# Kernel optimization log

Hardware: AMD Instinct MI355X
Metric: run time of the kernel (lower is better)

Reference implementation:

```python
import jax, jax.numpy as jnp
import numpy as np

H = 8          # kv heads
D = 128        # head dim
EPS = 1e-6
NEG = -1e9

def rmsnorm(x, w):
    rms = jnp.sqrt(jnp.mean(x * x, axis=-1, keepdims=True) + EPS)
    return x / rms * w

def apply_rotary(x, cos, sin):
    # x: [B, h, T, D]; cos/sin: [1, 1, T, D/2]
    x1, x2 = jnp.split(x, 2, axis=-1)
    return jnp.concatenate([x1 * cos - x2 * sin, x1 * sin + x2 * cos], axis=-1)


def setup_inputs() -> dict:
    key = jax.random.key(0)
    ks = jax.random.split(key, 7)
    B, T, hid = 1, 4096, 1024
    s = 0.02
    return {
        "x":   jax.random.normal(ks[0], (B, T, hid), jnp.float32),
        "cos": jax.random.normal(ks[1], (1, 1, T, D // 2), jnp.float32),
        "sin": jax.random.normal(ks[2], (1, 1, T, D // 2), jnp.float32),
        "Wq":  jax.random.normal(ks[3], (hid, 2 * hid), jnp.float32) * s,
        "Wk":  jax.random.normal(ks[4], (hid, hid), jnp.float32) * s,
        "Wv":  jax.random.normal(ks[5], (hid, hid), jnp.float32) * s,
        "Wo":  jax.random.normal(ks[6], (2 * hid, hid), jnp.float32) * s,
        "qn_w": jnp.ones((D,), jnp.float32),
        "kn_w": jnp.ones((D,), jnp.float32),
    }


def reference(x, cos, sin, Wq, Wk, Wv, Wo, qn_w, kn_w):
    B, T, _ = x.shape
    scale = D ** -0.5

    q = (x @ Wq).reshape(B, T, 2 * H, D).transpose(0, 2, 1, 3)  # [B,2H,T,D]
    k = (x @ Wk).reshape(B, T, H, D).transpose(0, 2, 1, 3)      # [B,H,T,D]
    v = (x @ Wv).reshape(B, T, H, D).transpose(0, 2, 1, 3)      # [B,H,T,D]

    q = apply_rotary(rmsnorm(q, qn_w), cos, sin)
    k = apply_rotary(rmsnorm(k, kn_w), cos, sin)

    # GQA expand: query head i uses kv head i // 2
    k = jnp.repeat(k, 2, axis=1)  # [B,2H,T,D]
    v = jnp.repeat(v, 2, axis=1)

    attn = jnp.einsum("bhtd,bhsd->bhts", q, k) * scale
    causal = jnp.tril(jnp.ones((T, T), bool))
    attn = jnp.where(causal, attn, NEG)
    attn = jax.nn.softmax(attn, axis=-1)

    out = jnp.einsum("bhts,bhsd->bhtd", attn, v)
    out = out.transpose(0, 2, 1, 3).reshape(B, T, 2 * H * D)
    return out @ Wo
```

## Files before the change

### kernel.cpp

```cpp
#include <hip/hip_runtime.h>
#include <hip/hip_bf16.h>

#define H2 16
#define HKV 8
#define DHEAD 128
#define HID 1024
#define NQ 2048

typedef unsigned short u16;
typedef __bf16 bf16x8 __attribute__((ext_vector_type(8)));
typedef float f32x4 __attribute__((ext_vector_type(4)));

__device__ __forceinline__ u16 f2bf(float x) {
    unsigned int u = __float_as_uint(x);
    unsigned int r = (u + 0x7fffu + ((u >> 16) & 1u)) >> 16;
    return (u16)r;
}

__device__ __forceinline__ unsigned int pack_bf16(float hi, float lo) {
    unsigned int a = __float_as_uint(hi) + 0x8000u;
    unsigned int b = __float_as_uint(lo) + 0x8000u;
    return __builtin_amdgcn_perm(a, b, 0x07060302u);
}

__device__ __forceinline__ bf16x8 ld_frag(const u16* p) {
    bf16x8 r;
    *reinterpret_cast<uint4*>(&r) = *reinterpret_cast<const uint4*>(p);
    return r;
}

__device__ __forceinline__ void gload_lds16(const u16* g, u16* l) {
    __builtin_amdgcn_global_load_lds((const __attribute__((address_space(1))) void*)g,
                                     (__attribute__((address_space(3))) void*)l, 16, 0, 0);
}

__global__ __launch_bounds__(256) void cast_f32_bf16(const float* __restrict__ in,
                                                     u16* __restrict__ out, int n4) {
    int i = blockIdx.x * 256 + threadIdx.x;
    if (i < n4) {
        float4 v = reinterpret_cast<const float4*>(in)[i];
        ushort4 o;
        o.x = f2bf(v.x); o.y = f2bf(v.y); o.z = f2bf(v.z); o.w = f2bf(v.w);
        reinterpret_cast<ushort4*>(out)[i] = o;
    }
}

__global__ __launch_bounds__(256) void transpose_cast(const float* __restrict__ in,
                                                      u16* __restrict__ out, int K, int N) {
    __shared__ u16 t[32][34];
    int k0 = blockIdx.x * 32, n0 = blockIdx.y * 32;
    for (int c = threadIdx.x; c < 1024; c += 256) {
        int k = c >> 5, n = c & 31;
        t[k][n] = f2bf(in[(size_t)(k0 + k) * N + n0 + n]);
    }
    __syncthreads();
    for (int c = threadIdx.x; c < 1024; c += 256) {
        int n = c >> 5, k = c & 31;
        out[(size_t)(n0 + n) * K + k0 + k] = t[k][n];
    }
}

__global__ __launch_bounds__(256) void gemm_bf16(const u16* __restrict__ A,
                                                 const u16* __restrict__ Bt,
                                                 float* __restrict__ C,
                                                 int M, int N, int K) {
    __shared__ u16 As[128 * 32];
    __shared__ u16 Bs[128 * 32];
    int tid = threadIdx.x;
    int lane = tid & 63, wave = tid >> 6;
    int quad = lane >> 4, l15 = lane & 15;
    int wr = wave >> 1, wc = wave & 1;
    int m0 = blockIdx.y * 128, n0 = blockIdx.x * 128;

    f32x4 zero = {0.f, 0.f, 0.f, 0.f};
    f32x4 acc[4][4];
    for (int i = 0; i < 4; i++)
        for (int j = 0; j < 4; j++) acc[i][j] = zero;

    int r0 = 16 * wave + (lane >> 2);
    int r1 = r0 + 64;
    int ks0 = (lane & 3) ^ ((r0 >> 1) & 3);
    int ks1 = (lane & 3) ^ ((r1 >> 1) & 3);
    const u16* ga0 = A + (size_t)(m0 + r0) * K + ks0 * 8;
    const u16* ga1 = A + (size_t)(m0 + r1) * K + ks1 * 8;
    const u16* gb0 = Bt + (size_t)(n0 + r0) * K + ks0 * 8;
    const u16* gb1 = Bt + (size_t)(n0 + r1) * K + ks1 * 8;
    u16* la0 = &As[wave * 512];
    u16* la1 = &As[(wave + 4) * 512];
    u16* lb0 = &Bs[wave * 512];
    u16* lb1 = &Bs[(wave + 4) * 512];

    int swz = (quad ^ ((l15 >> 1) & 3)) * 8;

    for (int k0 = 0; k0 < K; k0 += 32) {
        __syncthreads();
        gload_lds16(ga0 + k0, la0);
        gload_lds16(ga1 + k0, la1);
        gload_lds16(gb0 + k0, lb0);
        gload_lds16(gb1 + k0, lb1);
        __syncthreads();
        bf16x8 a[4], b[4];
        #pragma unroll
        for (int i = 0; i < 4; i++) a[i] = ld_frag(&As[(64 * wr + 16 * i + l15) * 32 + swz]);
        #pragma unroll
        for (int j = 0; j < 4; j++) b[j] = ld_frag(&Bs[(64 * wc + 16 * j + l15) * 32 + swz]);
        #pragma unroll
        for (int i = 0; i < 4; i++)
            #pragma unroll
            for (int j = 0; j < 4; j++)
                acc[i][j] = __builtin_amdgcn_mfma_f32_16x16x32_bf16(a[i], b[j], acc[i][j], 0, 0, 0);
    }
    for (int i = 0; i < 4; i++) {
        int rowb = m0 + 64 * wr + 16 * i + quad * 4;
        for (int j = 0; j < 4; j++) {
            int col = n0 + 64 * wc + 16 * j + l15;
            for (int r = 0; r < 4; r++)
                C[(size_t)(rowb + r) * N + col] = acc[i][j][r];
        }
    }
}

__global__ __launch_bounds__(256) void norm_rope(const float* __restrict__ raw,
                                                 const float* __restrict__ cosp,
                                                 const float* __restrict__ sinp,
                                                 const float* __restrict__ w,
                                                 u16* __restrict__ out,
                                                 int T, int nh, int rowstride, int coloff,
                                                 float outscale) {
    int wave = threadIdx.x >> 6, lane = threadIdx.x & 63;
    int wid = blockIdx.x * 4 + wave;
    int t = wid / nh, h = wid % nh;
    if (t >= T) return;
    const float* r = raw + (size_t)t * rowstride + coloff + h * 128;
    float v1 = r[lane], v2 = r[lane + 64];
    float ss = v1 * v1 + v2 * v2;
    for (int off = 1; off < 64; off <<= 1) ss += __shfl_xor(ss, off);
    float inv = rsqrtf(ss * (1.f / 128.f) + 1e-6f);
    float n1 = v1 * inv * w[lane], n2 = v2 * inv * w[lane + 64];
    float c = cosp[(size_t)t * 64 + lane], s = sinp[(size_t)t * 64 + lane];
    float o1 = (n1 * c - n2 * s) * outscale;
    float o2 = (n1 * s + n2 * c) * outscale;
    u16* op = out + ((size_t)h * T + t) * 128;
    op[lane] = f2bf(o1);
    op[lane + 64] = f2bf(o2);
}

__global__ __launch_bounds__(256) void v_transpose(const float* __restrict__ vraw,
                                                   u16* __restrict__ Vbt, int T) {
    __shared__ u16 tt[128][72];
    int h = blockIdx.y, t0 = blockIdx.x * 64;
    for (int c = threadIdx.x; c < 8192; c += 256) {
        int r = c >> 7, d = c & 127;
        tt[d][r] = f2bf(vraw[(size_t)(t0 + r) * 4096 + 3072 + h * 128 + d]);
    }
    __syncthreads();
    for (int c = threadIdx.x; c < 8192; c += 256) {
        int d = c >> 6, r = c & 63;
        Vbt[((size_t)h * 128 + d) * T + t0 + r] = tt[d][r];
    }
}

__global__ __launch_bounds__(256) void flash_attn(const u16* __restrict__ Qb,
                                                  const u16* __restrict__ Kb,
                                                  const u16* __restrict__ Vbt,
                                                  u16* __restrict__ attn, int T) {
    __shared__ u16 Ks[2][64 * 128];
    __shared__ u16 Vt[2][128 * 64];
    __shared__ u16 Ps[64 * 64];
    int tid = threadIdx.x;
    int lane = tid & 63, wave = tid >> 6;
    int quad = lane >> 4, l15 = lane & 15;
    int swb8 = (l15 & 7) * 8;
    int h = blockIdx.y;
    int j = (int)blockIdx.x;
    int kvh = h >> 1;

    const u16* kbase = Kb + (size_t)kvh * T * 128;
    const u16* vbase = Vbt + (size_t)kvh * 128 * T;

    int krow_ = (lane >> 4);
    int kseg_ = (lane & 15);
    int vrow_ = (lane >> 3);
    int vseg_ = (lane & 7);

    auto stage = [&](int s0, int b) {
        #pragma unroll
        for (int i = 0; i < 4; i++) {
            int ch = wave * 4 + i;
            int r = ch * 4 + krow_;
            int s = kseg_ ^ (r & 7);
            gload_lds16(kbase + (size_t)(s0 + r) * 128 + s * 8, &Ks[b][ch * 512]);
        }
        #pragma unroll
        for (int i = 0; i < 4; i++) {
            int ch = wave * 4 + i;
            int d = ch * 8 + vrow_;
            int s = vseg_ ^ (d & 7);
            gload_lds16(vbase + (size_t)d * T + s0 + s * 8, &Vt[b][ch * 512]);
        }
    };

    bf16x8 onesf;
    #pragma unroll
    for (int i = 0; i < 8; i++) onesf[i] = (__bf16)1.0f;
    f32x4 zero = {0.f, 0.f, 0.f, 0.f};
    const float L2E = 1.44269504f;

    for (int pass = 0; pass < 2; ++pass) {
        int qt = pass == 0 ? (63 - j) : j;
        int q0 = qt * 64;

        bf16x8 qf[4];
        {
            const u16* qp = Qb + ((size_t)h * T + q0 + 16 * wave + l15) * 128 + quad * 8;
            #pragma unroll
            for (int kk = 0; kk < 4; kk++) qf[kk] = ld_frag(qp + kk * 32);
        }

        float m_i = -3.0e38f;
        f32x4 lsum = zero;
        f32x4 o[8];
        for (int dt = 0; dt < 8; dt++) o[dt] = zero;

        int ntiles = qt + 1;
        stage(0, 0);
        __syncthreads();

        for (int it = 0; it < ntiles; ++it) {
            int b = it & 1;
            if (it + 1 < ntiles) stage((it + 1) * 64, 1 - b);
            int s0 = it * 64;

            f32x4 scT[4];
            for (int jt = 0; jt < 4; jt++) scT[jt] = zero;
            #pragma unroll
            for (int kk = 0; kk < 4; kk++)
                #pragma unroll
                for (int jt = 0; jt < 4; jt++) {
                    bf16x8 kfrag = ld_frag(&Ks[b][(jt * 16 + l15) * 128 + ((kk * 32 + quad * 8) ^ swb8)]);
                    scT[jt] = __builtin_amdgcn_mfma_f32_16x16x32_bf16(kfrag, qf[kk], scT[jt], 0, 0, 0);
                }

            if (s0 == q0) {
                int qloc = 16 * wave + l15;
                #pragma unroll
                for (int jt = 0; jt < 4; jt++)
                    for (int r = 0; r < 4; r++)
                        if (jt * 16 + quad * 4 + r > qloc) scT[jt][r] = -1e30f;
            }

            float mt = scT[0][0];
            #pragma unroll
            for (int jt = 0; jt < 4; jt++)
                for (int r = 0; r < 4; r++) mt = fmaxf(mt, scT[jt][r]);
            mt = fmaxf(mt, __shfl_xor(mt, 16));
            mt = fmaxf(mt, __shfl_xor(mt, 32));
            float mnew = fmaxf(m_i, mt);
            float alpha = __expf(m_i - mnew);
            m_i = mnew;
            float mls = mnew * L2E;

            #pragma unroll
            for (int jt = 0; jt < 4; jt++)
                for (int r = 0; r < 4; r++)
                    scT[jt][r] = exp2f(fmaf(scT[jt][r], L2E, -mls));

            {
                int prow = 16 * wave + l15;
                #pragma unroll
                for (int jt = 0; jt < 4; jt++) {
                    int s8 = 2 * jt + (quad >> 1);
                    uint2 wv;
                    wv.x = pack_bf16(scT[jt][1], scT[jt][0]);
                    wv.y = pack_bf16(scT[jt][3], scT[jt][2]);
                    *reinterpret_cast<uint2*>(&Ps[prow * 64 + (s8 ^ (l15 & 7)) * 8 + (quad & 1) * 4]) = wv;
                }
            }

            float av[4];
            #pragma unroll
            for (int r = 0; r < 4; r++) av[r] = __shfl(alpha, quad * 4 + r);
            #pragma unroll
            for (int r = 0; r < 4; r++) lsum[r] *= av[r];
            #pragma unroll
            for (int dt = 0; dt < 8; dt++)
                for (int r = 0; r < 4; r++) o[dt][r] *= av[r];

            asm volatile("s_waitcnt lgkmcnt(0)" ::: "memory");

            #pragma unroll
            for (int kk2 = 0; kk2 < 2; kk2++) {
                bf16x8 pa = ld_frag(&Ps[(16 * wave + l15) * 64 + (((4 * kk2 + quad) ^ (l15 & 7)) * 8)]);
                lsum = __builtin_amdgcn_mfma_f32_16x16x32_bf16(pa, onesf, lsum, 0, 0, 0);
                #pragma unroll
                for (int dt = 0; dt < 8; dt++) {
                    bf16x8 vb = ld_frag(&Vt[b][(dt * 16 + l15) * 64 + ((kk2 * 32 + quad * 8) ^ swb8)]);
                    o[dt] = __builtin_amdgcn_mfma_f32_16x16x32_bf16(pa, vb, o[dt], 0, 0, 0);
                }
            }
            __syncthreads();
        }

        float inv[4];
        for (int r = 0; r < 4; r++) inv[r] = 1.f / lsum[r];
        for (int dt = 0; dt < 8; dt++)
            for (int r = 0; r < 4; r++) {
                int row = q0 + 16 * wave + quad * 4 + r;
                attn[(size_t)row * NQ + h * DHEAD + dt * 16 + l15] = f2bf(o[dt][r] * inv[r]);
            }
    }
}

extern "C" void kernel_launch(void* const* d_in, const int* in_sizes, int n_in,
                              void* d_out, int out_size, void* d_ws, size_t ws_size,
                              hipStream_t stream) {
    const float* x    = (const float*)d_in[0];
    const float* cosp = (const float*)d_in[1];
    const float* sinp = (const float*)d_in[2];
    const float* Wq   = (const float*)d_in[3];
    const float* Wk   = (const float*)d_in[4];
    const float* Wv   = (const float*)d_in[5];
    const float* Wo   = (const float*)d_in[6];
    const float* qnw  = (const float*)d_in[7];
    const float* knw  = (const float*)d_in[8];
    float* out = (float*)d_out;
    const int T = in_sizes[1] / 64;

    char* ws = (char*)d_ws;
    size_t off = 0;
    auto alloc = [&](size_t bytes) {
        char* p = ws + off;
        off += (bytes + 255) & ~(size_t)255;
        return p;
    };
    u16*   xb     = (u16*)alloc((size_t)T * HID * 2);
    u16*   Wqkvb  = (u16*)alloc((size_t)4096 * HID * 2);
    u16*   Wob    = (u16*)alloc((size_t)HID * NQ * 2);
    float* qkvraw = (float*)alloc((size_t)T * 4096 * 4);
    u16*   Qb     = (u16*)alloc((size_t)H2 * T * DHEAD * 2);
    u16*   Kb     = (u16*)alloc((size_t)HKV * T * DHEAD * 2);
    u16*   Vbt    = (u16*)alloc((size_t)HKV * DHEAD * T * 2);
    u16*   attn   = (u16*)alloc((size_t)T * NQ * 2);

    cast_f32_bf16<<<(T * HID / 4 + 255) / 256, 256, 0, stream>>>(x, xb, T * HID / 4);
    transpose_cast<<<dim3(HID / 32, NQ / 32), 256, 0, stream>>>(Wq, Wqkvb, HID, NQ);
    transpose_cast<<<dim3(HID / 32, HID / 32), 256, 0, stream>>>(Wk, Wqkvb + (size_t)2048 * HID, HID, HID);
    transpose_cast<<<dim3(HID / 32, HID / 32), 256, 0, stream>>>(Wv, Wqkvb + (size_t)3072 * HID, HID, HID);
    transpose_cast<<<dim3(NQ / 32, HID / 32), 256, 0, stream>>>(Wo, Wob, NQ, HID);

    gemm_bf16<<<dim3(4096 / 128, T / 128), 256, 0, stream>>>(xb, Wqkvb, qkvraw, T, 4096, HID);

    const float scale = 0.08838834764831845f;
    norm_rope<<<T * H2 / 4, 256, 0, stream>>>(qkvraw, cosp, sinp, qnw, Qb, T, H2, 4096, 0, scale);
    norm_rope<<<T * HKV / 4, 256, 0, stream>>>(qkvraw, cosp, sinp, knw, Kb, T, HKV, 4096, 2048, 1.0f);
    v_transpose<<<dim3(T / 64, HKV), 256, 0, stream>>>(qkvraw, Vbt, T);

    flash_attn<<<dim3(32, H2), 256, 0, stream>>>(Qb, Kb, Vbt, attn, T);

    gemm_bf16<<<dim3(HID / 128, T / 128), 256, 0, stream>>>(attn, Wob, out, T, HID, NQ);
}
```

Baseline: 377.5 us.

## Emit bf16 QKV, merge norm/rope and weight casts, use 64-wide output GEMM tiles

The QKV projection now writes bf16 instead of fp32, which halves intermediate traffic. The downstream norm/rope and V transpose read bf16 directly, and the Q and K norm_rope launches are merged into one kernel. The Wk and Wv transpose-casts are fused into a single launch. The output projection uses a 128x64 tile so the N=1024 GEMM gets more blocks for better CU occupancy. Rounding QKV to bf16 before RMSNorm adds a small precision loss.

```diff
diff --git a/kernel.cpp b/kernel.cpp
--- a/kernel.cpp
+++ b/kernel.cpp
@@ -15,6 +15,9 @@
     unsigned int u = __float_as_uint(x);
     unsigned int r = (u + 0x7fffu + ((u >> 16) & 1u)) >> 16;
     return (u16)r;
+}
+__device__ __forceinline__ float bf2f(u16 x) {
+    return __uint_as_float(((unsigned int)x) << 16);
 }
 
 __device__ __forceinline__ unsigned int pack_bf16(float hi, float lo) {
@@ -48,6 +51,25 @@
 __global__ __launch_bounds__(256) void transpose_cast(const float* __restrict__ in,
                                                       u16* __restrict__ out, int K, int N) {
     __shared__ u16 t[32][34];
+    int k0 = blockIdx.x * 32, n0 = blockIdx.y * 32;
+    for (int c = threadIdx.x; c < 1024; c += 256) {
+        int k = c >> 5, n = c & 31;
+        t[k][n] = f2bf(in[(size_t)(k0 + k) * N + n0 + n]);
+    }
+    __syncthreads();
+    for (int c = threadIdx.x; c < 1024; c += 256) {
+        int n = c >> 5, k = c & 31;
+        out[(size_t)(n0 + n) * K + k0 + k] = t[k][n];
+    }
+}
+
+__global__ __launch_bounds__(256) void transpose_cast2(const float* __restrict__ inA,
+                                                       const float* __restrict__ inB,
+                                                       u16* __restrict__ outA,
+                                                       u16* __restrict__ outB, int K, int N) {
+    __shared__ u16 t[32][34];
+    const float* in = blockIdx.z ? inB : inA;
+    u16* out = blockIdx.z ? outB : outA;
     int k0 = blockIdx.x * 32, n0 = blockIdx.y * 32;
     for (int c = threadIdx.x; c < 1024; c += 256) {
         int k = c >> 5, n = c & 31;
@@ -120,19 +142,144 @@
     }
 }
 
-__global__ __launch_bounds__(256) void norm_rope(const float* __restrict__ raw,
-                                                 const float* __restrict__ cosp,
-                                                 const float* __restrict__ sinp,
-                                                 const float* __restrict__ w,
-                                                 u16* __restrict__ out,
-                                                 int T, int nh, int rowstride, int coloff,
-                                                 float outscale) {
+__global__ __launch_bounds__(256) void gemm_bf16_ob(const u16* __restrict__ A,
+                                                    const u16* __restrict__ Bt,
+                                                    u16* __restrict__ C,
+                                                    int M, int N, int K) {
+    __shared__ u16 As[128 * 32];
+    __shared__ u16 Bs[128 * 32];
+    int tid = threadIdx.x;
+    int lane = tid & 63, wave = tid >> 6;
+    int quad = lane >> 4, l15 = lane & 15;
+    int wr = wave >> 1, wc = wave & 1;
+    int m0 = blockIdx.y * 128, n0 = blockIdx.x * 128;
+
+    f32x4 zero = {0.f, 0.f, 0.f, 0.f};
+    f32x4 acc[4][4];
+    for (int i = 0; i < 4; i++)
+        for (int j = 0; j < 4; j++) acc[i][j] = zero;
+
+    int r0 = 16 * wave + (lane >> 2);
+    int r1 = r0 + 64;
+    int ks0 = (lane & 3) ^ ((r0 >> 1) & 3);
+    int ks1 = (lane & 3) ^ ((r1 >> 1) & 3);
+    const u16* ga0 = A + (size_t)(m0 + r0) * K + ks0 * 8;
+    const u16* ga1 = A + (size_t)(m0 + r1) * K + ks1 * 8;
+    const u16* gb0 = Bt + (size_t)(n0 + r0) * K + ks0 * 8;
+    const u16* gb1 = Bt + (size_t)(n0 + r1) * K + ks1 * 8;
+    u16* la0 = &As[wave * 512];
+    u16* la1 = &As[(wave + 4) * 512];
+    u16* lb0 = &Bs[wave * 512];
+    u16* lb1 = &Bs[(wave + 4) * 512];
+
+    int swz = (quad ^ ((l15 >> 1) & 3)) * 8;
+
+    for (int k0 = 0; k0 < K; k0 += 32) {
+        __syncthreads();
+        gload_lds16(ga0 + k0, la0);
+        gload_lds16(ga1 + k0, la1);
+        gload_lds16(gb0 + k0, lb0);
+        gload_lds16(gb1 + k0, lb1);
+        __syncthreads();
+        bf16x8 a[4], b[4];
+        #pragma unroll
+        for (int i = 0; i < 4; i++) a[i] = ld_frag(&As[(64 * wr + 16 * i + l15) * 32 + swz]);
+        #pragma unroll
+        for (int j = 0; j < 4; j++) b[j] = ld_frag(&Bs[(64 * wc + 16 * j + l15) * 32 + swz]);
+        #pragma unroll
+        for (int i = 0; i < 4; i++)
+            #pragma unroll
+            for (int j = 0; j < 4; j++)
+                acc[i][j] = __builtin_amdgcn_mfma_f32_16x16x32_bf16(a[i], b[j], acc[i][j], 0, 0, 0);
+    }
+    for (int i = 0; i < 4; i++) {
+        int rowb = m0 + 64 * wr + 16 * i + quad * 4;
+        for (int j = 0; j < 4; j++) {
+            int col = n0 + 64 * wc + 16 * j + l15;
+            for (int r = 0; r < 4; r++)
+                C[(size_t)(rowb + r) * N + col] = f2bf(acc[i][j][r]);
+        }
+    }
+}
+
+__global__ __launch_bounds__(256) void gemm_bf16_n64(const u16* __restrict__ A,
+                                                     const u16* __restrict__ Bt,
+                                                     float* __restrict__ C,
+                                                     int M, int N, int K) {
+    __shared__ u16 As[128 * 32];
+    __shared__ u16 Bs[64 * 32];
+    int tid = threadIdx.x;
+    int lane = tid & 63, wave = tid >> 6;
+    int quad = lane >> 4, l15 = lane & 15;
+    int m0 = blockIdx.y * 128, n0 = blockIdx.x * 64;
+
+    f32x4 zero = {0.f, 0.f, 0.f, 0.f};
+    f32x4 acc[2][4];
+    for (int i = 0; i < 2; i++)
+        for (int j = 0; j < 4; j++) acc[i][j] = zero;
+
+    int ra0 = 32 * wave + (lane >> 2);
+    int ra1 = ra0 + 16;
+    int rb  = 16 * wave + (lane >> 2);
+    int ksa0 = (lane & 3) ^ ((ra0 >> 1) & 3);
+    int ksa1 = (lane & 3) ^ ((ra1 >> 1) & 3);
+    int ksb  = (lane & 3) ^ ((rb >> 1) & 3);
+    const u16* ga0 = A + (size_t)(m0 + ra0) * K + ksa0 * 8;
+    const u16* ga1 = A + (size_t)(m0 + ra1) * K + ksa1 * 8;
+    const u16* gb  = Bt + (size_t)(n0 + rb) * K + ksb * 8;
+    u16* la0 = &As[(2 * wave) * 512];
+    u16* la1 = &As[(2 * wave + 1) * 512];
+    u16* lb  = &Bs[wave * 512];
+
+    int swz = (quad ^ ((l15 >> 1) & 3)) * 8;
+
+    for (int k0 = 0; k0 < K; k0 += 32) {
+        __syncthreads();
+        gload_lds16(ga0 + k0, la0);
+        gload_lds16(ga1 + k0, la1);
+        gload_lds16(gb + k0, lb);
+        __syncthreads();
+        bf16x8 a[2], b[4];
+        #pragma unroll
+        for (int i = 0; i < 2; i++) a[i] = ld_frag(&As[(32 * wave + 16 * i + l15) * 32 + swz]);
+        #pragma unroll
+        for (int j = 0; j < 4; j++) b[j] = ld_frag(&Bs[(16 * j + l15) * 32 + swz]);
+        #pragma unroll
+        for (int i = 0; i < 2; i++)
+            #pragma unroll
+            for (int j = 0; j < 4; j++)
+                acc[i][j] = __builtin_amdgcn_mfma_f32_16x16x32_bf16(a[i], b[j], acc[i][j], 0, 0, 0);
+    }
+    for (int i = 0; i < 2; i++) {
+        int rowb = m0 + 32 * wave + 16 * i + quad * 4;
+        for (int j = 0; j < 4; j++) {
+            int col = n0 + 16 * j + l15;
+            for (int r = 0; r < 4; r++)
+                C[(size_t)(rowb + r) * N + col] = acc[i][j][r];
+        }
+    }
+}
+
+__global__ __launch_bounds__(256) void norm_rope_qk(const u16* __restrict__ qkv,
+                                                    const float* __restrict__ cosp,
+                                                    const float* __restrict__ sinp,
+                                                    const float* __restrict__ qnw,
+                                                    const float* __restrict__ knw,
+                                                    u16* __restrict__ Qb,
+                                                    u16* __restrict__ Kb,
+                                                    int T, float qscale) {
     int wave = threadIdx.x >> 6, lane = threadIdx.x & 63;
     int wid = blockIdx.x * 4 + wave;
-    int t = wid / nh, h = wid % nh;
+    int t = wid / 24, unit = wid % 24;
     if (t >= T) return;
-    const float* r = raw + (size_t)t * rowstride + coloff + h * 128;
-    float v1 = r[lane], v2 = r[lane + 64];
+    bool isq = unit < 16;
+    int coloff = isq ? unit * 128 : 2048 + (unit - 16) * 128;
+    const float* w = isq ? qnw : knw;
+    float outscale = isq ? qscale : 1.0f;
+    u16* out = isq ? (Qb + ((size_t)unit * T + t) * 128)
+                   : (Kb + ((size_t)(unit - 16) * T + t) * 128);
+    const u16* r = qkv + (size_t)t * 4096 + coloff;
+    float v1 = bf2f(r[lane]), v2 = bf2f(r[lane + 64]);
     float ss = v1 * v1 + v2 * v2;
     for (int off = 1; off < 64; off <<= 1) ss += __shfl_xor(ss, off);
     float inv = rsqrtf(ss * (1.f / 128.f) + 1e-6f);
@@ -140,18 +287,17 @@
     float c = cosp[(size_t)t * 64 + lane], s = sinp[(size_t)t * 64 + lane];
     float o1 = (n1 * c - n2 * s) * outscale;
     float o2 = (n1 * s + n2 * c) * outscale;
-    u16* op = out + ((size_t)h * T + t) * 128;
-    op[lane] = f2bf(o1);
-    op[lane + 64] = f2bf(o2);
-}
-
-__global__ __launch_bounds__(256) void v_transpose(const float* __restrict__ vraw,
+    out[lane] = f2bf(o1);
+    out[lane + 64] = f2bf(o2);
+}
+
+__global__ __launch_bounds__(256) void v_transpose(const u16* __restrict__ qkv,
                                                    u16* __restrict__ Vbt, int T) {
     __shared__ u16 tt[128][72];
     int h = blockIdx.y, t0 = blockIdx.x * 64;
     for (int c = threadIdx.x; c < 8192; c += 256) {
         int r = c >> 7, d = c & 127;
-        tt[d][r] = f2bf(vraw[(size_t)(t0 + r) * 4096 + 3072 + h * 128 + d]);
+        tt[d][r] = qkv[(size_t)(t0 + r) * 4096 + 3072 + h * 128 + d];
     }
     __syncthreads();
     for (int c = threadIdx.x; c < 8192; c += 256) {
@@ -336,7 +482,7 @@
     u16*   xb     = (u16*)alloc((size_t)T * HID * 2);
     u16*   Wqkvb  = (u16*)alloc((size_t)4096 * HID * 2);
     u16*   Wob    = (u16*)alloc((size_t)HID * NQ * 2);
-    float* qkvraw = (float*)alloc((size_t)T * 4096 * 4);
+    u16*   qkvb   = (u16*)alloc((size_t)T * 4096 * 2);
     u16*   Qb     = (u16*)alloc((size_t)H2 * T * DHEAD * 2);
     u16*   Kb     = (u16*)alloc((size_t)HKV * T * DHEAD * 2);
     u16*   Vbt    = (u16*)alloc((size_t)HKV * DHEAD * T * 2);
@@ -344,18 +490,17 @@
 
     cast_f32_bf16<<<(T * HID / 4 + 255) / 256, 256, 0, stream>>>(x, xb, T * HID / 4);
     transpose_cast<<<dim3(HID / 32, NQ / 32), 256, 0, stream>>>(Wq, Wqkvb, HID, NQ);
-    transpose_cast<<<dim3(HID / 32, HID / 32), 256, 0, stream>>>(Wk, Wqkvb + (size_t)2048 * HID, HID, HID);
-    transpose_cast<<<dim3(HID / 32, HID / 32), 256, 0, stream>>>(Wv, Wqkvb + (size_t)3072 * HID, HID, HID);
+    transpose_cast2<<<dim3(HID / 32, HID / 32, 2), 256, 0, stream>>>(
+        Wk, Wv, Wqkvb + (size_t)2048 * HID, Wqkvb + (size_t)3072 * HID, HID, HID);
     transpose_cast<<<dim3(NQ / 32, HID / 32), 256, 0, stream>>>(Wo, Wob, NQ, HID);
 
-    gemm_bf16<<<dim3(4096 / 128, T / 128), 256, 0, stream>>>(xb, Wqkvb, qkvraw, T, 4096, HID);
+    gemm_bf16_ob<<<dim3(4096 / 128, T / 128), 256, 0, stream>>>(xb, Wqkvb, qkvb, T, 4096, HID);
 
     const float scale = 0.08838834764831845f;
-    norm_rope<<<T * H2 / 4, 256, 0, stream>>>(qkvraw, cosp, sinp, qnw, Qb, T, H2, 4096, 0, scale);
-    norm_rope<<<T * HKV / 4, 256, 0, stream>>>(qkvraw, cosp, sinp, knw, Kb, T, HKV, 4096, 2048, 1.0f);
-    v_transpose<<<dim3(T / 64, HKV), 256, 0, stream>>>(qkvraw, Vbt, T);
+    norm_rope_qk<<<T * 24 / 4, 256, 0, stream>>>(qkvb, cosp, sinp, qnw, knw, Qb, Kb, T, scale);
+    v_transpose<<<dim3(T / 64, HKV), 256, 0, stream>>>(qkvb, Vbt, T);
 
     flash_attn<<<dim3(32, H2), 256, 0, stream>>>(Qb, Kb, Vbt, attn, T);
 
-    gemm_bf16<<<dim3(HID / 128, T / 128), 256, 0, stream>>>(attn, Wob, out, T, HID, NQ);
-}
+    gemm_bf16_n64<<<dim3(HID / 64, T / 128), 256, 0, stream>>>(attn, Wob, out, T, HID, NQ);
+}
```

New measurement: 364.9 us. 1.03x faster.
